# Optimization experiments

Measured on AMD Instinct MI355X. Metric: run time of the kernel, lower is better.

The kernel has to match this reference:

```python
import jax, jax.numpy as jnp
import numpy as np

DEG = [1, 72, 201, 816, 1790, 3756, 6923, 12768, 20286, 31710, 51623, 82296, 124280, 177576, 251115, 326064, 395760, 456840, 506179, 516200, 507003, 493746, 489256, 453936, 420025, 411320, 427761, 420700, 420500, 426780, 414284, 407008, 394053, 360910, 322245, 313704, 282902, 270940, 237783, 209000, 193766, 177870, 162110, 144848, 121230, 112700, 93483, 88512, 72275, 80700, 68799, 56784, 42665, 30996, 25630, 12936, 9804, 8584, 5251, 3480, 3111, 2728, 1890, 1472, 1235, 330, 201, 68, 69, 0, 71]
_d = np.array(DEG, dtype=np.float64)
AVG_LOG = float((np.log(np.arange(len(_d)) + 1.0) * _d).sum() / _d.sum())  # avg_deg['log']

N_NODES, N_EDGES, N_GRAPHS = 10000, 100000, 64
TOWERS, F, F_OUT, N_LAYERS = 5, 75, 15, 4


def setup_inputs() -> dict:
    key = jax.random.key(0)
    ks = jax.random.split(key, 32)
    r = lambda i, shape: jax.random.normal(ks[i], shape, jnp.float32) * 0.1
    return {
        "x": jax.random.normal(ks[0], (N_NODES, 14), jnp.float32),
        "edge_index": jax.random.randint(ks[1], (2, N_EDGES), 0, N_NODES, dtype=jnp.int32),
        "edge_attr": jax.random.normal(ks[2], (N_EDGES, 4), jnp.float32),
        "batch": jnp.sort(jax.random.randint(ks[3], (N_NODES,), 0, N_GRAPHS, dtype=jnp.int32)),
        "node_emb_w": r(4, (14, F)), "node_emb_b": r(5, (F,)),
        "edge_emb_w": r(6, (4, 50)), "edge_emb_b": r(7, (50,)),
        "ee_w": r(8, (N_LAYERS, 50, F)), "ee_b": r(9, (N_LAYERS, F)),
        "pre_w": r(10, (N_LAYERS, TOWERS, 3 * F, F)), "pre_b": r(11, (N_LAYERS, TOWERS, F)),
        "post_w": r(12, (N_LAYERS, TOWERS, 13 * F, F_OUT)), "post_b": r(13, (N_LAYERS, TOWERS, F_OUT)),
        "lin_w": r(14, (N_LAYERS, F, F)), "lin_b": r(15, (N_LAYERS, F)),
        "bn_g": jnp.ones((N_LAYERS, F), jnp.float32), "bn_b": jnp.zeros((N_LAYERS, F), jnp.float32),
        "mlp_w1": r(16, (F, 50)), "mlp_b1": r(17, (50,)),
        "mlp_w2": r(18, (50, 25)), "mlp_b2": r(19, (25,)),
        "mlp_w3": r(20, (25, 1)), "mlp_b3": r(21, (1,)),
    }


def _pna_conv(x, src, dst, ea, ee_w, ee_b, pre_w, pre_b, post_w, post_b, lin_w, lin_b):
    # x: [N, F]; ea: [E, edge_dim]; divide_input=False so every tower sees full F.
    N = x.shape[0]
    e = ea @ ee_w + ee_b                                   # edge_encoder  [E, F]
    h = jnp.concatenate([x[dst], x[src], e], axis=-1)       # [x_i, x_j, e] [E, 3F]
    m = jnp.einsum('ef,tfg->etg', h, pre_w) + pre_b         # per-tower pre nn [E, T, F]
    cnt = jax.ops.segment_sum(jnp.ones((m.shape[0],), x.dtype), dst, N)  # in-degree [N]
    cnt1 = jnp.maximum(cnt, 1.0)[:, None, None]
    mean = jax.ops.segment_sum(m, dst, N) / cnt1
    mean_sq = jax.ops.segment_sum(m * m, dst, N) / cnt1
    std = jnp.sqrt(jax.nn.relu(mean_sq - mean * mean) + 1e-5)
    has = (cnt > 0)[:, None, None]
    mn = jnp.where(has, jax.ops.segment_min(m, dst, N), 0.0)
    mx = jnp.where(has, jax.ops.segment_max(m, dst, N), 0.0)
    agg = jnp.concatenate([mean, mn, mx, std], axis=-1)     # [N, T, 4F]
    scl = jnp.log(cnt1 + 1.0) / AVG_LOG                     # amplification scaler
    out = jnp.concatenate([agg, agg * scl, agg / scl], -1)  # identity/amp/atten [N, T, 12F]
    x_rep = jnp.broadcast_to(x[:, None, :], (N, TOWERS, x.shape[1]))
    out = jnp.concatenate([x_rep, out], axis=-1)            # [N, T, 13F]
    out = jnp.einsum('ntf,tfg->ntg', out, post_w) + post_b  # per-tower post nn [N, T, F_out]
    return out.reshape(N, -1) @ lin_w + lin_b               # [N, F]


def _bn(x, g, b):
    mu = x.mean(0)
    var = x.var(0)  # biased, as torch BatchNorm1d uses for normalization
    return (x - mu) * jax.lax.rsqrt(var + 1e-5) * g + b


def reference(x, edge_index, edge_attr, batch, node_emb_w, node_emb_b, edge_emb_w, edge_emb_b,
              ee_w, ee_b, pre_w, pre_b, post_w, post_b, lin_w, lin_b, bn_g, bn_b,
              mlp_w1, mlp_b1, mlp_w2, mlp_b2, mlp_w3, mlp_b3):
    src, dst = edge_index[0], edge_index[1]
    h = x @ node_emb_w + node_emb_b
    ea = edge_attr @ edge_emb_w + edge_emb_b
    for i in range(N_LAYERS):
        h = jax.nn.relu(_bn(_pna_conv(h, src, dst, ea, ee_w[i], ee_b[i], pre_w[i], pre_b[i],
                                      post_w[i], post_b[i], lin_w[i], lin_b[i]), bn_g[i], bn_b[i]))
    per_atom = h
    g = jax.ops.segment_sum(h, batch, N_GRAPHS)             # global_add_pool [G, F]
    g = jax.nn.relu(g @ mlp_w1 + mlp_b1)
    g = jax.nn.relu(g @ mlp_w2 + mlp_b2)
    g = (g @ mlp_w3 + mlp_b3).reshape(-1)                   # num_out==1 -> view(-1)
    return (g, per_atom)
```

## Files before the change

kernel.cpp:

```cpp
#include <hip/hip_runtime.h>
#include <math.h>

#define NN 10000
#define NE 100000
#define NGR 64
#define NT 5
#define FD 75
#define FOUT 15
#define NLAY 4
#define MAXB 1792

typedef __bf16 bf16;
typedef __bf16 bf16x8 __attribute__((ext_vector_type(8)));
typedef float f32x4 __attribute__((ext_vector_type(4)));

__device__ inline unsigned pk2(float a, float b) {
  bf16 x = (bf16)a, y = (bf16)b;
  unsigned short ux, uy;
  __builtin_memcpy(&ux, &x, 2); __builtin_memcpy(&uy, &y, 2);
  return (unsigned)ux | ((unsigned)uy << 16);
}


__global__ __launch_bounds__(256) void k_node_emb(const float* __restrict__ x,
    const float* __restrict__ w, const float* __restrict__ b, bf16* __restrict__ hbf) {
  int idx = blockIdx.x * 256 + threadIdx.x;
  if (idx >= NN * FD) return;
  int n = idx / FD, f = idx - n * FD;
  float acc = b[f];
#pragma unroll
  for (int k = 0; k < 14; ++k) acc += x[n * 14 + k] * w[k * FD + f];
  hbf[n * 80 + f] = (bf16)acc;
}

__global__ __launch_bounds__(256) void k_edge4(const float* __restrict__ eattr,
    bf16* __restrict__ eabf4) {
  int idx = blockIdx.x * 256 + threadIdx.x;
  if (idx >= NE * 8) return;
  int e = idx >> 3, c = idx & 7;
  eabf4[idx] = (c < 4) ? (bf16)eattr[e * 4 + c] : (bf16)0.f;
}

__global__ __launch_bounds__(256) void k_count(const int* __restrict__ dst, int* __restrict__ deg) {
  int e = blockIdx.x * 256 + threadIdx.x;
  if (e < NE) atomicAdd(&deg[dst[e]], 1);
}

__global__ __launch_bounds__(1024) void k_scan(const int* __restrict__ deg, int* __restrict__ rowptr) {
  __shared__ int buf[1024];
  __shared__ int carry;
  int tid = threadIdx.x;
  if (tid == 0) carry = 0;
  __syncthreads();
  for (int base = 0; base < NN; base += 1024) {
    int i = base + tid;
    int v = (i < NN) ? deg[i] : 0;
    buf[tid] = v;
    __syncthreads();
    for (int off = 1; off < 1024; off <<= 1) {
      int t = (tid >= off) ? buf[tid - off] : 0;
      __syncthreads();
      buf[tid] += t;
      __syncthreads();
    }
    int inc = buf[tid];
    int tot = buf[1023];
    if (i < NN) rowptr[i + 1] = carry + inc;
    __syncthreads();
    if (tid == 0) carry += tot;
    __syncthreads();
  }
  if (tid == 0) rowptr[0] = 0;
}

__global__ __launch_bounds__(256) void k_scl(const int* __restrict__ deg, float* __restrict__ scl,
                                             float* __restrict__ iscl, float inv_avg_log) {
  int n = blockIdx.x * 256 + threadIdx.x;
  if (n >= NN) return;
  float c1 = fmaxf((float)deg[n], 1.f);
  float s = logf(c1 + 1.f) * inv_avg_log;
  scl[n] = s;
  iscl[n] = 1.f / s;
}

__global__ __launch_bounds__(256) void k_scatter(const int* __restrict__ dst, const int* __restrict__ rowptr,
    int* __restrict__ cursor, int* __restrict__ eids) {
  int e = blockIdx.x * 256 + threadIdx.x;
  if (e >= NE) return;
  int d = dst[e];
  int pos = rowptr[d] + atomicAdd(&cursor[d], 1);
  eids[pos] = e;
}

__global__ __launch_bounds__(256) void k_next(const int* __restrict__ rowptr, int* __restrict__ nxt) {
  int n = blockIdx.x * 256 + threadIdx.x;
  if (n >= NN) return;
  int base = rowptr[n];
  int lo = n + 1, hi = min(n + 128, NN);
  while (lo < hi) {
    int mid = (lo + hi + 1) >> 1;
    if (rowptr[mid] - base <= 128) lo = mid; else hi = mid - 1;
  }
  nxt[n] = lo;
}

__global__ __launch_bounds__(1024) void k_walk(const int* __restrict__ nxt,
    int* __restrict__ bstart, int* __restrict__ nblk) {
  __shared__ int lnx[NN];
  int tid = threadIdx.x;
  for (int i = tid; i < NN; i += 1024) lnx[i] = nxt[i];
  __syncthreads();
  if (tid == 0) {
    int b = 0, n = 0;
    while (n < NN && b < MAXB) { bstart[b++] = n; n = lnx[n]; }
    bstart[b] = NN;
    nblk[0] = b;
  }
}


__global__ __launch_bounds__(256) void k_W12(const float* __restrict__ ew,
    const float* __restrict__ ebias, const float* __restrict__ ee_wA, const float* __restrict__ ee_bA,
    float* __restrict__ W12A, float* __restrict__ bcombA) {
  const int l = blockIdx.y;
  const float* ee_w = ee_wA + (size_t)l * 50 * FD;
  const float* ee_b = ee_bA + (size_t)l * FD;
  int idx = blockIdx.x * 256 + threadIdx.x;
  if (idx >= 375) return;
  if (idx < 300) {
    int d = idx / 75, o = idx - d * 75;
    float v = 0.f;
    for (int j = 0; j < 50; ++j) v += ew[d * 50 + j] * ee_w[j * 75 + o];
    W12A[(size_t)l * 300 + idx] = v;
  } else {
    int o = idx - 300;
    float v = ee_b[o];
    for (int j = 0; j < 50; ++j) v += ebias[j] * ee_w[j * 75 + o];
    bcombA[(size_t)l * 80 + o] = v;
  }
}

__global__ __launch_bounds__(256) void k_combine(const float* __restrict__ pre_wA,
    const float* __restrict__ pre_bA, const float* __restrict__ W12A, const float* __restrict__ bcombA,
    bf16* __restrict__ WctA, float* __restrict__ bcA) {
  const int l = blockIdx.y;
  const float* pre_w = pre_wA + (size_t)l * NT * 225 * FD;
  const float* pre_b = pre_bA + (size_t)l * NT * FD;
  const float* W12   = W12A + (size_t)l * 300;
  const float* bcomb = bcombA + (size_t)l * 80;
  bf16* Wct = WctA + (size_t)l * 384 * 192;
  float* bc = bcA + (size_t)l * 384;
  int idx = blockIdx.x * 256 + threadIdx.x;
  if (idx >= 384 * 192) return;
  int c = idx / 192, s = idx - c * 192;
  int t = c / 75, g = c - t * 75;
  int chunk = s >> 6, within = s & 63, sblk = within >> 3, elem = within & 7;
  int lb = sblk ^ (c & 7);
  int k = chunk * 64 + lb * 8 + elem;
  float v = 0.f;
  if (c < 375) {
    if (k < 75)                    v = pre_w[(t * 225 + k) * 75 + g];
    else if (k >= 80 && k < 155)   v = pre_w[(t * 225 + 75 + (k - 80)) * 75 + g];
    else if (k >= 160 && k < 164) {
      int d = k - 160;
      float a = 0.f;
      for (int f2 = 0; f2 < 75; ++f2) a += W12[d * 75 + f2] * pre_w[(t * 225 + 150 + f2) * 75 + g];
      v = a;
    }
  }
  Wct[c * 192 + s] = (bf16)v;
  if (s == 0) {
    float a = 0.f;
    if (c < 375) {
      a = pre_b[t * 75 + g];
      for (int f2 = 0; f2 < 75; ++f2) a += bcomb[f2] * pre_w[(t * 225 + 150 + f2) * 75 + g];
    }
    bc[c] = a;
  }
}

__global__ __launch_bounds__(256) void k_PL(const float* __restrict__ pwA,
    const float* __restrict__ lwA, float* __restrict__ PLA) {
  const int l = blockIdx.y;
  const float* pw = pwA + (size_t)l * NT * 975 * FOUT;
  const float* lw = lwA + (size_t)l * FD * FD;
  float* PL = PLA + (size_t)l * 5 * 975 * 80;
  int idx = blockIdx.x * 256 + threadIdx.x;
  if (idx >= 5 * 975 * 80) return;
  int t = idx / (975 * 80), rem = idx - t * 975 * 80;
  int row = rem / 80, o = rem - row * 80;
  float v = 0.f;
  if (o < 75) {
#pragma unroll
    for (int j = 0; j < 15; ++j)
      v += pw[((size_t)t * 975 + row) * 15 + j] * lw[(t * 15 + j) * 75 + o];
  }
  PL[idx] = v;
}

__global__ __launch_bounds__(256) void k_combine2b(const float* __restrict__ PLA,
    bf16* __restrict__ Wct2A) {
  const int l = blockIdx.y;
  const float* PL = PLA + (size_t)l * 5 * 975 * 80;
  bf16* Wct2 = Wct2A + (size_t)l * 256 * 1664;
  int idx = blockIdx.x * 256 + threadIdx.x;
  if (idx >= 256 * 1664) return;
  int c = idx / 1664, s = idx - c * 1664;
  int chunk = s >> 6, within = s & 63, sblk = within >> 3, elem = within & 7;
  int lb = sblk ^ (c & 7);
  int k = chunk * 64 + lb * 8 + elem;
  int g2 = c / 80, o = c - g2 * 80;
  float val = 0.f;
  if (c < 240 && o < 75) {
    if (k < 75) {
      if (g2 == 0) {
#pragma unroll
        for (int t = 0; t < 5; ++t) val += PL[(t * 975 + k) * 80 + o];
      }
    } else if (k >= 80 && k < 1616) {
      int q = k - 80;
      int si = q / 384, cc = q - si * 384;
      if (cc < 375) {
        int t = cc / 75, g = cc - t * 75;
        int row = 75 + g2 * 300 + si * 75 + g;
        val = PL[((size_t)t * 975 + row) * 80 + o];
      }
    }
  }
  Wct2[(size_t)c * 1664 + s] = (bf16)val;
}

__global__ __launch_bounds__(128) void k_zbias(const float* __restrict__ pbA,
    const float* __restrict__ lwA, const float* __restrict__ lbA, float* __restrict__ zbA) {
  const int l = blockIdx.y;
  const float* pb = pbA + (size_t)l * NT * FOUT;
  const float* lw = lwA + (size_t)l * FD * FD;
  const float* lb = lbA + (size_t)l * FD;
  float* zb = zbA + (size_t)l * 80;
  int o = threadIdx.x;
  if (o >= 80) return;
  float val = 0.f;
  if (o < 75) {
    val = lb[o];
    for (int t = 0; t < 5; ++t)
      for (int j = 0; j < 15; ++j)
        val += pb[t * 15 + j] * lw[(t * 15 + j) * 75 + o];
  }
  zb[o] = val;
}


#define APTR_(g_, pd_, ps_, pe_) \
  ((g_) < 10 ? (pd_) + (g_) * 8 : (g_) < 20 ? (ps_) + ((g_) - 10) * 8 : \
   (g_) < 21 ? (pe_) : zerobuf)

#define LOADA(c_) do { int g_ = (c_) * 8 + slb;                \
    pa0 = *(const uint4*)APTR_(g_, pd0, ps0, pe0);             \
    pa1 = *(const uint4*)APTR_(g_, pd1, ps1, pe1);             \
    pa2 = *(const uint4*)APTR_(g_, pd2, ps2, pe2);             \
    pa3 = *(const uint4*)APTR_(g_, pd3, ps3, pe3); } while (0)

#define LOADB(ntb_, c_) do {                                                      \
    const bf16* wp_ = Wct + (size_t)((ntb_) + sr) * 192 + (c_) * 64 + slb * 8;    \
    pq0 = *(const uint4*)(wp_ + 0 * 6144);                                        \
    pq1 = *(const uint4*)(wp_ + 1 * 6144);                                        \
    pq2 = *(const uint4*)(wp_ + 2 * 6144);                                        \
    pq3 = *(const uint4*)(wp_ + 3 * 6144); } while (0)

#define STORE_AB() do { int swz_ = (slb ^ (sr & 7)) << 4;       \
    *(uint4*)(As + (0 * 32 + sr) * 128 + swz_) = pa0;           \
    *(uint4*)(As + (1 * 32 + sr) * 128 + swz_) = pa1;           \
    *(uint4*)(As + (2 * 32 + sr) * 128 + swz_) = pa2;           \
    *(uint4*)(As + (3 * 32 + sr) * 128 + swz_) = pa3;           \
    *(uint4*)(Bs + (0 * 32 + sr) * 128 + (slb << 4)) = pq0;     \
    *(uint4*)(Bs + (1 * 32 + sr) * 128 + (slb << 4)) = pq1;     \
    *(uint4*)(Bs + (2 * 32 + sr) * 128 + (slb << 4)) = pq2;     \
    *(uint4*)(Bs + (3 * 32 + sr) * 128 + (slb << 4)) = pq3; } while (0)

__global__ __launch_bounds__(256) void k_pre_fused(
    const bf16* __restrict__ hbf, const bf16* __restrict__ eabf4,
    const int* __restrict__ eids, const int* __restrict__ srcA, const int* __restrict__ dstA,
    const int* __restrict__ rowptr, const int* __restrict__ bstart, const int* __restrict__ nblk,
    const bf16* __restrict__ Wct, const float* __restrict__ bc,
    const bf16* __restrict__ zerobuf, bf16* __restrict__ aggbf2) {
  __shared__ __align__(16) unsigned char smem[33792];
  unsigned char* As = smem;
  unsigned char* Bs = smem + 16384;
  bf16* m_lds = (bf16*)smem;
  __shared__ const bf16* pDl[128];
  __shared__ const bf16* pSl[128];
  __shared__ const bf16* pEl[128];
  __shared__ int nodeRows[129];
  __shared__ int nq[5];

  const int b = blockIdx.x;
  if (b >= nblk[0]) return;
  const int ntb = blockIdx.y * 128;
  const int tid = threadIdx.x;
  const int n0b = bstart[b], n1b = bstart[b + 1];
  const int rbase = rowptr[n0b];
  const int nrows = rowptr[n1b] - rbase;
  const int nnod = n1b - n0b;

  if (tid == 0) { nq[0] = 0; nq[1] = 0; nq[2] = 0; nq[3] = 0; nq[4] = nnod; }
  if (tid < 128) {
    if (tid < nrows) {
      int e = eids[rbase + tid];
      pDl[tid] = hbf + dstA[e] * 80;
      pSl[tid] = hbf + srcA[e] * 80;
      pEl[tid] = eabf4 + e * 8;
    } else { pDl[tid] = zerobuf; pSl[tid] = zerobuf; pEl[tid] = zerobuf; }
  }
  if (tid <= nnod) nodeRows[tid] = rowptr[n0b + tid] - rbase;
  __syncthreads();
  if (tid < nnod) {
#pragma unroll
    for (int q = 1; q <= 3; ++q) {
      int target = (nrows * q) >> 2;
      if (nodeRows[tid] < target && nodeRows[tid + 1] >= target) nq[q] = tid + 1;
    }
  }

  const int lane = tid & 63;
  const int wave = tid >> 6;
  const int wr = wave >> 1, wc = wave & 1;
  const int l15 = lane & 15, l4 = lane >> 4;
  const int sr = tid >> 3, slb = tid & 7;

  const bf16 *pd0 = pDl[sr],      *ps0 = pSl[sr],      *pe0 = pEl[sr];
  const bf16 *pd1 = pDl[32 + sr], *ps1 = pSl[32 + sr], *pe1 = pEl[32 + sr];
  const bf16 *pd2 = pDl[64 + sr], *ps2 = pSl[64 + sr], *pe2 = pEl[64 + sr];
  const bf16 *pd3 = pDl[96 + sr], *ps3 = pSl[96 + sr], *pe3 = pEl[96 + sr];

  f32x4 acc[4][4];
  f32x4 zv = {0.f, 0.f, 0.f, 0.f};
#pragma unroll
  for (int i = 0; i < 4; ++i)
#pragma unroll
    for (int j = 0; j < 4; ++j) acc[i][j] = zv;

  uint4 pa0, pa1, pa2, pa3, pq0, pq1, pq2, pq3;
  LOADA(0); LOADB(ntb, 0);

#pragma unroll
  for (int c = 0; c < 3; ++c) {
    STORE_AB();
    __syncthreads();
    if (c < 2) { LOADA(c + 1); LOADB(ntb, c + 1); }
#pragma unroll
    for (int kk = 0; kk < 2; ++kk) {
      int kb = kk * 4 + l4;
      bf16x8 af[4], bfv[4];
#pragma unroll
      for (int i = 0; i < 4; ++i) {
        int row = wr * 64 + i * 16 + l15;
        af[i] = *(const bf16x8*)(As + row * 128 + ((kb ^ (row & 7)) << 4));
      }
#pragma unroll
      for (int j = 0; j < 4; ++j) {
        int col = wc * 64 + j * 16 + l15;
        bfv[j] = *(const bf16x8*)(Bs + col * 128 + ((kb ^ (col & 7)) << 4));
      }
#pragma unroll
      for (int i = 0; i < 4; ++i)
#pragma unroll
        for (int j = 0; j < 4; ++j)
          acc[i][j] = __builtin_amdgcn_mfma_f32_16x16x32_bf16(af[i], bfv[j], acc[i][j], 0, 0, 0);
    }
    __syncthreads();
  }

  float bcv[4];
#pragma unroll
  for (int j = 0; j < 4; ++j) bcv[j] = bc[ntb + wc * 64 + j * 16 + l15];
#pragma unroll
  for (int i = 0; i < 4; ++i) {
    int R = wr * 64 + i * 16 + l4 * 4;
#pragma unroll
    for (int j = 0; j < 4; ++j) {
      int col = wc * 64 + j * 16 + l15;
#pragma unroll
      for (int q = 0; q < 4; ++q)
        m_lds[(R + q) * 132 + col] = (bf16)(acc[i][j][q] + bcv[j]);
    }
  }
  __syncthreads();

  {
    const int cp = tid & 63;
    const int qq = tid >> 6;
    const unsigned char* mb = (const unsigned char*)m_lds;
    for (int i = nq[qq]; i < nq[qq + 1]; ++i) {
      int ra = nodeRows[i], rb2 = nodeRows[i + 1];
      float s0 = 0.f, q0 = 0.f, a0 = INFINITY, b0 = -INFINITY;
      float s1 = 0.f, q1 = 0.f, a1 = INFINITY, b1 = -INFINITY;
      for (int r = ra; r < rb2; ++r) {
        unsigned u = *(const unsigned*)(mb + r * 264 + cp * 4);
        float v0 = __uint_as_float(u << 16);
        float v1 = __uint_as_float(u & 0xffff0000u);
        s0 += v0; q0 += v0 * v0; a0 = fminf(a0, v0); b0 = fmaxf(b0, v0);
        s1 += v1; q1 += v1 * v1; a1 = fminf(a1, v1); b1 = fmaxf(b1, v1);
      }
      int d = rb2 - ra;
      float inv = 1.f / ((d > 0) ? (float)d : 1.f);
      float m0 = s0 * inv, m1 = s1 * inv;
      float sd0 = sqrtf(fmaxf(q0 * inv - m0 * m0, 0.f) + 1e-5f);
      float sd1 = sqrtf(fmaxf(q1 * inv - m1 * m1, 0.f) + 1e-5f);
      if (d == 0) { a0 = 0.f; b0 = 0.f; a1 = 0.f; b1 = 0.f; }
      bf16* ag = aggbf2 + (size_t)(n0b + i) * 1536 + ntb + cp * 2;
      *(unsigned*)(ag)        = pk2(m0, m1);
      *(unsigned*)(ag + 384)  = pk2(a0, a1);
      *(unsigned*)(ag + 768)  = pk2(b0, b1);
      *(unsigned*)(ag + 1152) = pk2(sd0, sd1);
    }
  }
}


#define APG_(g_) ((nA >= NN || (g_) >= 202) ? zerobuf : \
    ((g_) < 10 ? hbf + nA * 80 + (g_) * 8 : aggbf2 + (size_t)nA * 1536 + ((g_) - 10) * 8))

#define LOADP4(c_) do {                                                 \
    int gA_ = (c_) * 16 + slb;                                          \
    pa0 = *(const uint4*)APG_(gA_);                                     \
    pa1 = *(const uint4*)APG_(gA_ + 8);                                 \
    int ko_ = (c_) * 128 + slb * 8;                                     \
    pb0 = *(const uint4*)(pc0 + ko_);                                   \
    pb1 = *(const uint4*)(pc0 + ko_ + 64);                              \
    pb2 = *(const uint4*)(pc1 + ko_);                                   \
    pb3 = *(const uint4*)(pc1 + ko_ + 64);                              \
    pb4 = *(const uint4*)(pc2 + ko_);                                   \
    pb5 = *(const uint4*)(pc2 + ko_ + 64);                              \
    pb6 = *(const uint4*)(pc3 + ko_);                                   \
    pb7 = *(const uint4*)(pc3 + ko_ + 64);                              \
  } while (0)

__global__ __launch_bounds__(256) void k_post4(const bf16* __restrict__ hbf,
    const bf16* __restrict__ aggbf2, const bf16* __restrict__ Wct2,
    const float* __restrict__ zb, const float* __restrict__ scl, const float* __restrict__ iscl,
    const bf16* __restrict__ zerobuf, float* __restrict__ z, float* __restrict__ stat_raw_l) {
  __shared__ __align__(16) unsigned char smem[40960];
  unsigned char* As = smem;
  unsigned char* Bs = smem + 8192;
  float* Ps = (float*)smem;
  __shared__ float sclS[32], isclS[32];
  const int n0 = blockIdx.x * 32;
  const int y  = blockIdx.y;
  const int tid = threadIdx.x;
  const int lane = tid & 63, wave = tid >> 6;
  const int l15 = lane & 15, l4 = lane >> 4;
  const int sr = tid >> 3, slb = tid & 7;
  const int nA = n0 + sr;

  const bf16 *pc0, *pc1, *pc2, *pc3;
  {
    int c0 = sr, c1 = sr + 32, c2 = sr + 64, c3 = sr + 96;
    int l0 = (c0 / 40) * 80 + y * 40 + (c0 % 40);
    int l1 = (c1 / 40) * 80 + y * 40 + (c1 % 40);
    int l2 = (c2 / 40) * 80 + y * 40 + (c2 % 40);
    int l3 = (c3 < 120) ? ((c3 / 40) * 80 + y * 40 + (c3 % 40)) : 0;
    pc0 = Wct2 + (size_t)l0 * 1664;
    pc1 = Wct2 + (size_t)l1 * 1664;
    pc2 = Wct2 + (size_t)l2 * 1664;
    pc3 = Wct2 + (size_t)l3 * 1664;
  }
  if (tid < 32) {
    int n = n0 + tid;
    sclS[tid] = (n < NN) ? scl[n] : 0.f;
    isclS[tid] = (n < NN) ? iscl[n] : 0.f;
  }

  f32x4 acc[2][2];
  f32x4 zvv = {0.f, 0.f, 0.f, 0.f};
#pragma unroll
  for (int i = 0; i < 2; ++i)
#pragma unroll
    for (int j = 0; j < 2; ++j) acc[i][j] = zvv;

  uint4 pa0, pa1, pb0, pb1, pb2, pb3, pb4, pb5, pb6, pb7;
  LOADP4(0);
  for (int c = 0; c < 13; ++c) {
    {
      int s1_ = (slb ^ (sr & 7)) << 4;
      *(uint4*)(As + sr * 256 + s1_) = pa0;
      *(uint4*)(As + sr * 256 + s1_ + 128) = pa1;
      *(uint4*)(Bs + (sr)      * 256 + (slb << 4)) = pb0;
      *(uint4*)(Bs + (sr)      * 256 + (slb << 4) + 128) = pb1;
      *(uint4*)(Bs + (sr + 32) * 256 + (slb << 4)) = pb2;
      *(uint4*)(Bs + (sr + 32) * 256 + (slb << 4) + 128) = pb3;
      *(uint4*)(Bs + (sr + 64) * 256 + (slb << 4)) = pb4;
      *(uint4*)(Bs + (sr + 64) * 256 + (slb << 4) + 128) = pb5;
      *(uint4*)(Bs + (sr + 96) * 256 + (slb << 4)) = pb6;
      *(uint4*)(Bs + (sr + 96) * 256 + (slb << 4) + 128) = pb7;
    }
    __syncthreads();
    if (c < 12) LOADP4(c + 1);
#pragma unroll
    for (int kk = 0; kk < 4; ++kk) {
      int kb = kk * 4 + l4;
      bf16x8 af[2], bv[2];
#pragma unroll
      for (int i = 0; i < 2; ++i) {
        int row = i * 16 + l15;
        af[i] = *(const bf16x8*)(As + row * 256 + (((kb & 8) | ((kb & 7) ^ (row & 7))) << 4));
      }
#pragma unroll
      for (int j = 0; j < 2; ++j) {
        int cidx = wave * 32 + j * 16 + l15;
        bv[j] = *(const bf16x8*)(Bs + cidx * 256 + (((kb & 8) | ((kb & 7) ^ (cidx & 7))) << 4));
      }
#pragma unroll
      for (int i = 0; i < 2; ++i)
#pragma unroll
        for (int j = 0; j < 2; ++j)
          acc[i][j] = __builtin_amdgcn_mfma_f32_16x16x32_bf16(af[i], bv[j], acc[i][j], 0, 0, 0);
    }
    __syncthreads();
  }

#pragma unroll
  for (int i = 0; i < 2; ++i) {
#pragma unroll
    for (int j = 0; j < 2; ++j) {
      int cidx = wave * 32 + j * 16 + l15;
#pragma unroll
      for (int q = 0; q < 4; ++q)
        Ps[(i * 16 + l4 * 4 + q) * 132 + cidx] = acc[i][j][q];
    }
  }
  __syncthreads();

  float v0_, v1_, v2_, v3_, v4_;
  int r0_, r1_, r2_, r3_, r4_, f0_, f1_, f2_, f3_, f4_;
#define EPI(t_, vv_, rr_, ff_) do {                                           \
    int idx_ = tid + (t_) * 256;                                              \
    rr_ = idx_ / 40; ff_ = idx_ - rr_ * 40;                                   \
    int n_ = n0 + rr_, zc_ = y * 40 + ff_;                                    \
    float v_ = 0.f;                                                           \
    if (n_ < NN && zc_ < 75) {                                                \
      v_ = Ps[rr_ * 132 + ff_] + sclS[rr_] * Ps[rr_ * 132 + 40 + ff_]         \
         + isclS[rr_] * Ps[rr_ * 132 + 80 + ff_] + zb[zc_];                   \
      z[n_ * 75 + zc_] = v_;                                                  \
    }                                                                         \
    vv_ = v_;                                                                 \
  } while (0)
  EPI(0, v0_, r0_, f0_); EPI(1, v1_, r1_, f1_); EPI(2, v2_, r2_, f2_);
  EPI(3, v3_, r3_, f3_); EPI(4, v4_, r4_, f4_);
#undef EPI
  __syncthreads();
  Ps[r0_ * 132 + f0_] = v0_;
  Ps[r1_ * 132 + f1_] = v1_;
  Ps[r2_ * 132 + f2_] = v2_;
  Ps[r3_ * 132 + f3_] = v3_;
  Ps[r4_ * 132 + f4_] = v4_;
  __syncthreads();
  if (tid < 40) {
    int zc = y * 40 + tid;
    if (zc < 75) {
      float s = 0.f, s2 = 0.f;
#pragma unroll
      for (int r = 0; r < 32; ++r) {
        float v = Ps[r * 132 + tid];
        s += v; s2 += v * v;
      }
      atomicAdd(&stat_raw_l[zc], s);
      atomicAdd(&stat_raw_l[75 + zc], s2);
    }
  }
}

__global__ __launch_bounds__(256) void k_bnapply(const float* __restrict__ z,
    const float* __restrict__ stat_raw, const float* __restrict__ g, const float* __restrict__ b,
    float* __restrict__ outF, bf16* __restrict__ hbf) {
  int idx = blockIdx.x * 256 + threadIdx.x;
  if (idx >= NN * FD) return;
  int n = idx / FD, f = idx - n * FD;
  float mu = stat_raw[f] * (1.f / NN);
  float var = stat_raw[75 + f] * (1.f / NN) - mu * mu;
  var = fmaxf(var, 0.f);
  float rs = 1.f / sqrtf(var + 1e-5f);
  float v = (z[idx] - mu) * rs * g[f] + b[f];
  v = fmaxf(v, 0.f);
  if (outF) outF[idx] = v;
  hbf[n * 80 + f] = (bf16)v;
}

__global__ __launch_bounds__(256) void k_pool(const float* __restrict__ h, const int* __restrict__ batch,
                                              float* __restrict__ gpool) {
  int idx = blockIdx.x * 256 + threadIdx.x;
  if (idx >= NN * FD) return;
  int n = idx / FD, f = idx - n * FD;
  atomicAdd(&gpool[batch[n] * FD + f], h[idx]);
}

__global__ __launch_bounds__(256) void k_mlp(const float* __restrict__ gpool,
    const float* __restrict__ w1, const float* __restrict__ b1,
    const float* __restrict__ w2, const float* __restrict__ b2,
    const float* __restrict__ w3, const float* __restrict__ b3,
    float* __restrict__ out) {
  __shared__ float G[NGR * FD];
  __shared__ float G1[NGR * 50];
  __shared__ float G2[NGR * 25];
  int tid = threadIdx.x;
  for (int i = tid; i < NGR * FD; i += 256) G[i] = gpool[i];
  __syncthreads();
  for (int i = tid; i < NGR * 50; i += 256) {
    int r = i / 50, c = i - r * 50;
    float a = b1[c];
    for (int k = 0; k < FD; ++k) a += G[r * FD + k] * w1[k * 50 + c];
    G1[i] = fmaxf(a, 0.f);
  }
  __syncthreads();
  for (int i = tid; i < NGR * 25; i += 256) {
    int r = i / 25, c = i - r * 25;
    float a = b2[c];
    for (int k = 0; k < 50; ++k) a += G1[r * 50 + k] * w2[k * 25 + c];
    G2[i] = fmaxf(a, 0.f);
  }
  __syncthreads();
  if (tid < NGR) {
    float a = b3[0];
    for (int k = 0; k < 25; ++k) a += G2[tid * 25 + k] * w3[k];
    out[tid] = a;
  }
}


extern "C" void kernel_launch(void* const* d_in, const int* in_sizes, int n_in,
                              void* d_out, int out_size, void* d_ws, size_t ws_size,
                              hipStream_t stream) {
  (void)in_sizes; (void)n_in; (void)out_size; (void)ws_size;
  const float* x      = (const float*)d_in[0];
  const int*   eidx   = (const int*)  d_in[1];
  const float* eattr  = (const float*)d_in[2];
  const int*   batch  = (const int*)  d_in[3];
  const float* nw     = (const float*)d_in[4];
  const float* nb     = (const float*)d_in[5];
  const float* ew     = (const float*)d_in[6];
  const float* ebias  = (const float*)d_in[7];
  const float* ee_w   = (const float*)d_in[8];
  const float* ee_b   = (const float*)d_in[9];
  const float* pre_w  = (const float*)d_in[10];
  const float* pre_b  = (const float*)d_in[11];
  const float* post_w = (const float*)d_in[12];
  const float* post_b = (const float*)d_in[13];
  const float* lin_w  = (const float*)d_in[14];
  const float* lin_b  = (const float*)d_in[15];
  const float* bn_g   = (const float*)d_in[16];
  const float* bn_b   = (const float*)d_in[17];
  const float* w1 = (const float*)d_in[18];
  const float* b1 = (const float*)d_in[19];
  const float* w2 = (const float*)d_in[20];
  const float* b2 = (const float*)d_in[21];
  const float* w3 = (const float*)d_in[22];
  const float* b3 = (const float*)d_in[23];

  const int* srcA = eidx;
  const int* dstA = eidx + NE;

  char* base = (char*)d_ws;
  size_t off = 0;
  auto alloc = [&](size_t bytes) -> char* {
    char* p = base + off;
    off = (off + bytes + 255) & ~(size_t)255;
    return p;
  };
  bf16*  hbf    = (bf16*) alloc((size_t)NN * 80 * 2);
  bf16*  eabf4  = (bf16*) alloc((size_t)NE * 8 * 2);
  bf16*  aggbf2 = (bf16*) alloc((size_t)NN * 1536 * 2);
  float* z      = (float*)alloc((size_t)NN * FD * 4);
  bf16*  WctA   = (bf16*) alloc((size_t)NLAY * 384 * 192 * 2);
  float* bcA    = (float*)alloc((size_t)NLAY * 384 * 4);
  bf16*  Wct2A  = (bf16*) alloc((size_t)NLAY * 256 * 1664 * 2);
  float* zbA    = (float*)alloc((size_t)NLAY * 80 * 4);
  float* PLA    = (float*)alloc((size_t)NLAY * 5 * 975 * 80 * 4);
  float* W12A   = (float*)alloc((size_t)NLAY * 300 * 4);
  float* bcombA = (float*)alloc((size_t)NLAY * 80 * 4);
  float* scl    = (float*)alloc(NN * 4);
  float* iscl   = (float*)alloc(NN * 4);
  int*   deg    = (int*)alloc(NN * 4);
  int*   rowptr = (int*)alloc((NN + 1) * 4);
  int*   cursor = (int*)alloc(NN * 4);
  int*   eids   = (int*)alloc(NE * 4);
  int*   nxt    = (int*)alloc(NN * 4);
  int*   bstart = (int*)alloc((MAXB + 1) * 4);
  int*   nblk   = (int*)alloc(16);
  float* stat_all = (float*)alloc((size_t)NLAY * 160 * 4);
  float* gpool  = (float*)alloc(NGR * FD * 4);
  bf16*  zerobuf = (bf16*)alloc(256);

  static const int DEG_TAB[71] = {1, 72, 201, 816, 1790, 3756, 6923, 12768, 20286, 31710,
    51623, 82296, 124280, 177576, 251115, 326064, 395760, 456840, 506179, 516200, 507003,
    493746, 489256, 453936, 420025, 411320, 427761, 420700, 420500, 426780, 414284, 407008,
    394053, 360910, 322245, 313704, 282902, 270940, 237783, 209000, 193766, 177870, 162110,
    144848, 121230, 112700, 93483, 88512, 72275, 80700, 68799, 56784, 42665, 30996, 25630,
    12936, 9804, 8584, 5251, 3480, 3111, 2728, 1890, 1472, 1235, 330, 201, 68, 69, 0, 71};
  double num = 0.0, den = 0.0;
  for (int i = 0; i < 71; ++i) { num += log((double)i + 1.0) * DEG_TAB[i]; den += DEG_TAB[i]; }
  float inv_avg_log = (float)(den / num);

  hipMemsetAsync(deg, 0, NN * 4, stream);
  hipMemsetAsync(cursor, 0, NN * 4, stream);
  hipMemsetAsync(gpool, 0, NGR * FD * 4, stream);
  hipMemsetAsync(stat_all, 0, (size_t)NLAY * 160 * 4, stream);
  hipMemsetAsync(zerobuf, 0, 256, stream);

  k_node_emb<<<(NN * FD + 255) / 256, 256, 0, stream>>>(x, nw, nb, hbf);
  k_edge4<<<(NE * 8 + 255) / 256, 256, 0, stream>>>(eattr, eabf4);
  k_count<<<(NE + 255) / 256, 256, 0, stream>>>(dstA, deg);
  k_scan<<<1, 1024, 0, stream>>>(deg, rowptr);
  k_scl<<<(NN + 255) / 256, 256, 0, stream>>>(deg, scl, iscl, inv_avg_log);
  k_scatter<<<(NE + 255) / 256, 256, 0, stream>>>(dstA, rowptr, cursor, eids);
  k_next<<<(NN + 255) / 256, 256, 0, stream>>>(rowptr, nxt);
  k_walk<<<1, 1024, 0, stream>>>(nxt, bstart, nblk);

  {
    dim3 gw(2, NLAY);
    k_W12<<<gw, 256, 0, stream>>>(ew, ebias, ee_w, ee_b, W12A, bcombA);
    dim3 gc((384 * 192 + 255) / 256, NLAY);
    k_combine<<<gc, 256, 0, stream>>>(pre_w, pre_b, W12A, bcombA, WctA, bcA);
    dim3 gp((5 * 975 * 80 + 255) / 256, NLAY);
    k_PL<<<gp, 256, 0, stream>>>(post_w, lin_w, PLA);
    dim3 g2((256 * 1664 + 255) / 256, NLAY);
    k_combine2b<<<g2, 256, 0, stream>>>(PLA, Wct2A);
    dim3 gz(1, NLAY);
    k_zbias<<<gz, 128, 0, stream>>>(post_b, lin_w, lin_b, zbA);
  }

  float* outp = (float*)d_out;
  for (int l = 0; l < NLAY; ++l) {
    dim3 gpref(MAXB, 3);
    k_pre_fused<<<gpref, 256, 0, stream>>>(hbf, eabf4, eids, srcA, dstA, rowptr, bstart, nblk,
        WctA + (size_t)l * 384 * 192, bcA + (size_t)l * 384, zerobuf, aggbf2);
    dim3 gpost((NN + 31) / 32, 2);
    k_post4<<<gpost, 256, 0, stream>>>(hbf, aggbf2, Wct2A + (size_t)l * 256 * 1664,
        zbA + (size_t)l * 80, scl, iscl, zerobuf, z, stat_all + (size_t)l * 160);
    float* wdst = (l == NLAY - 1) ? (outp + NGR) : nullptr;
    k_bnapply<<<(NN * FD + 255) / 256, 256, 0, stream>>>(z, stat_all + (size_t)l * 160,
        bn_g + (size_t)l * FD, bn_b + (size_t)l * FD, wdst, hbf);
  }

  k_pool<<<(NN * FD + 255) / 256, 256, 0, stream>>>(outp + NGR, batch, gpool);
  k_mlp<<<1, 256, 0, stream>>>(gpool, w1, b1, w2, b2, w3, b3, outp);
}
```

Measured before the change: 568.6 us.

## Load gathered A operands directly from global into MFMA registers, skip LDS staging

The pre-aggregation GEMM no longer stages the gathered dst/src/edge rows through shared memory. Each lane computes byte offsets into hbf and the edge buffer and loads its bf16x8 A fragments straight from global memory. B tiles are double-buffered in LDS instead, which removes one barrier and the LDS round-trip for A. A pad-zeroing kernel is added so the 75..79 columns of hbf are zero, since the K layout now reads those padding slots directly. The trade-off is uncoalesced per-lane global loads for A, and edge offsets are relative to hbf, which relies on unsigned offset arithmetic.

Result: faster. 545.0 us (-4.2%).

```diff
diff --git a/kernel.cpp b/kernel.cpp
--- a/kernel.cpp
+++ b/kernel.cpp
@@ -31,6 +31,13 @@
 #pragma unroll
   for (int k = 0; k < 14; ++k) acc += x[n * 14 + k] * w[k * FD + f];
   hbf[n * 80 + f] = (bf16)acc;
+}
+
+__global__ __launch_bounds__(256) void k_hpad(bf16* __restrict__ hbf) {
+  int idx = blockIdx.x * 256 + threadIdx.x;
+  if (idx >= NN * 5) return;
+  int n = idx / 5, f = 75 + idx % 5;
+  hbf[n * 80 + f] = (bf16)0.f;
 }
 
 __global__ __launch_bounds__(256) void k_edge4(const float* __restrict__ eattr,
@@ -250,16 +257,6 @@
 }
 
 
-#define APTR_(g_, pd_, ps_, pe_) \
-  ((g_) < 10 ? (pd_) + (g_) * 8 : (g_) < 20 ? (ps_) + ((g_) - 10) * 8 : \
-   (g_) < 21 ? (pe_) : zerobuf)
-
-#define LOADA(c_) do { int g_ = (c_) * 8 + slb;                \
-    pa0 = *(const uint4*)APTR_(g_, pd0, ps0, pe0);             \
-    pa1 = *(const uint4*)APTR_(g_, pd1, ps1, pe1);             \
-    pa2 = *(const uint4*)APTR_(g_, pd2, ps2, pe2);             \
-    pa3 = *(const uint4*)APTR_(g_, pd3, ps3, pe3); } while (0)
-
 #define LOADB(ntb_, c_) do {                                                      \
     const bf16* wp_ = Wct + (size_t)((ntb_) + sr) * 192 + (c_) * 64 + slb * 8;    \
     pq0 = *(const uint4*)(wp_ + 0 * 6144);                                        \
@@ -267,29 +264,51 @@
     pq2 = *(const uint4*)(wp_ + 2 * 6144);                                        \
     pq3 = *(const uint4*)(wp_ + 3 * 6144); } while (0)
 
-#define STORE_AB() do { int swz_ = (slb ^ (sr & 7)) << 4;       \
-    *(uint4*)(As + (0 * 32 + sr) * 128 + swz_) = pa0;           \
-    *(uint4*)(As + (1 * 32 + sr) * 128 + swz_) = pa1;           \
-    *(uint4*)(As + (2 * 32 + sr) * 128 + swz_) = pa2;           \
-    *(uint4*)(As + (3 * 32 + sr) * 128 + swz_) = pa3;           \
-    *(uint4*)(Bs + (0 * 32 + sr) * 128 + (slb << 4)) = pq0;     \
-    *(uint4*)(Bs + (1 * 32 + sr) * 128 + (slb << 4)) = pq1;     \
-    *(uint4*)(Bs + (2 * 32 + sr) * 128 + (slb << 4)) = pq2;     \
-    *(uint4*)(Bs + (3 * 32 + sr) * 128 + (slb << 4)) = pq3; } while (0)
+#define STOREB(BS_) do {                                          \
+    *(uint4*)((BS_) + (0 * 32 + sr) * 128 + (slb << 4)) = pq0;    \
+    *(uint4*)((BS_) + (1 * 32 + sr) * 128 + (slb << 4)) = pq1;    \
+    *(uint4*)((BS_) + (2 * 32 + sr) * 128 + (slb << 4)) = pq2;    \
+    *(uint4*)((BS_) + (3 * 32 + sr) * 128 + (slb << 4)) = pq3; } while (0)
+
+#define DO_KK(BS_, KB_, A0_, A1_, A2_, A3_) do {                         \
+    bf16x8 af0 = *(const bf16x8*)(A0_);                                  \
+    bf16x8 af1 = *(const bf16x8*)(A1_);                                  \
+    bf16x8 af2 = *(const bf16x8*)(A2_);                                  \
+    bf16x8 af3 = *(const bf16x8*)(A3_);                                  \
+    const unsigned char* bp_ = (BS_) + (((KB_) ^ (l15 & 7)) << 4) + wc * 8192 + l15 * 128; \
+    bf16x8 bv0 = *(const bf16x8*)(bp_ + 0 * 2048);                       \
+    bf16x8 bv1 = *(const bf16x8*)(bp_ + 1 * 2048);                       \
+    bf16x8 bv2 = *(const bf16x8*)(bp_ + 2 * 2048);                       \
+    bf16x8 bv3 = *(const bf16x8*)(bp_ + 3 * 2048);                       \
+    acc[0][0] = __builtin_amdgcn_mfma_f32_16x16x32_bf16(af0, bv0, acc[0][0], 0, 0, 0); \
+    acc[1][0] = __builtin_amdgcn_mfma_f32_16x16x32_bf16(af1, bv0, acc[1][0], 0, 0, 0); \
+    acc[2][0] = __builtin_amdgcn_mfma_f32_16x16x32_bf16(af2, bv0, acc[2][0], 0, 0, 0); \
+    acc[3][0] = __builtin_amdgcn_mfma_f32_16x16x32_bf16(af3, bv0, acc[3][0], 0, 0, 0); \
+    acc[0][1] = __builtin_amdgcn_mfma_f32_16x16x32_bf16(af0, bv1, acc[0][1], 0, 0, 0); \
+    acc[1][1] = __builtin_amdgcn_mfma_f32_16x16x32_bf16(af1, bv1, acc[1][1], 0, 0, 0); \
+    acc[2][1] = __builtin_amdgcn_mfma_f32_16x16x32_bf16(af2, bv1, acc[2][1], 0, 0, 0); \
+    acc[3][1] = __builtin_amdgcn_mfma_f32_16x16x32_bf16(af3, bv1, acc[3][1], 0, 0, 0); \
+    acc[0][2] = __builtin_amdgcn_mfma_f32_16x16x32_bf16(af0, bv2, acc[0][2], 0, 0, 0); \
+    acc[1][2] = __builtin_amdgcn_mfma_f32_16x16x32_bf16(af1, bv2, acc[1][2], 0, 0, 0); \
+    acc[2][2] = __builtin_amdgcn_mfma_f32_16x16x32_bf16(af2, bv2, acc[2][2], 0, 0, 0); \
+    acc[3][2] = __builtin_amdgcn_mfma_f32_16x16x32_bf16(af3, bv2, acc[3][2], 0, 0, 0); \
+    acc[0][3] = __builtin_amdgcn_mfma_f32_16x16x32_bf16(af0, bv3, acc[0][3], 0, 0, 0); \
+    acc[1][3] = __builtin_amdgcn_mfma_f32_16x16x32_bf16(af1, bv3, acc[1][3], 0, 0, 0); \
+    acc[2][3] = __builtin_amdgcn_mfma_f32_16x16x32_bf16(af2, bv3, acc[2][3], 0, 0, 0); \
+    acc[3][3] = __builtin_amdgcn_mfma_f32_16x16x32_bf16(af3, bv3, acc[3][3], 0, 0, 0); \
+  } while (0)
 
 __global__ __launch_bounds__(256) void k_pre_fused(
-    const bf16* __restrict__ hbf, const bf16* __restrict__ eabf4,
-    const int* __restrict__ eids, const int* __restrict__ srcA, const int* __restrict__ dstA,
+    const bf16* __restrict__ hbf, const int* __restrict__ eids,
+    const int* __restrict__ srcA, const int* __restrict__ dstA,
     const int* __restrict__ rowptr, const int* __restrict__ bstart, const int* __restrict__ nblk,
     const bf16* __restrict__ Wct, const float* __restrict__ bc,
-    const bf16* __restrict__ zerobuf, bf16* __restrict__ aggbf2) {
+    bf16* __restrict__ aggbf2, unsigned eoff_base) {
   __shared__ __align__(16) unsigned char smem[33792];
-  unsigned char* As = smem;
-  unsigned char* Bs = smem + 16384;
+  unsigned char* Bs0 = smem;
+  unsigned char* Bs1 = smem + 16384;
   bf16* m_lds = (bf16*)smem;
-  __shared__ const bf16* pDl[128];
-  __shared__ const bf16* pSl[128];
-  __shared__ const bf16* pEl[128];
+  __shared__ unsigned dOffL[128], sOffL[128], eOffL[128];
   __shared__ int nodeRows[129];
   __shared__ int nq[5];
 
@@ -304,12 +323,10 @@
 
   if (tid == 0) { nq[0] = 0; nq[1] = 0; nq[2] = 0; nq[3] = 0; nq[4] = nnod; }
   if (tid < 128) {
-    if (tid < nrows) {
-      int e = eids[rbase + tid];
-      pDl[tid] = hbf + dstA[e] * 80;
-      pSl[tid] = hbf + srcA[e] * 80;
-      pEl[tid] = eabf4 + e * 8;
-    } else { pDl[tid] = zerobuf; pSl[tid] = zerobuf; pEl[tid] = zerobuf; }
+    int e = (tid < nrows) ? eids[rbase + tid] : 0;
+    dOffL[tid] = (unsigned)(dstA[e] * 160);
+    sOffL[tid] = (unsigned)(srcA[e] * 160);
+    eOffL[tid] = eoff_base + (unsigned)(e * 16);
   }
   if (tid <= nnod) nodeRows[tid] = rowptr[n0b + tid] - rbase;
   __syncthreads();
@@ -327,10 +344,11 @@
   const int l15 = lane & 15, l4 = lane >> 4;
   const int sr = tid >> 3, slb = tid & 7;
 
-  const bf16 *pd0 = pDl[sr],      *ps0 = pSl[sr],      *pe0 = pEl[sr];
-  const bf16 *pd1 = pDl[32 + sr], *ps1 = pSl[32 + sr], *pe1 = pEl[32 + sr];
-  const bf16 *pd2 = pDl[64 + sr], *ps2 = pSl[64 + sr], *pe2 = pEl[64 + sr];
-  const bf16 *pd3 = pDl[96 + sr], *ps3 = pSl[96 + sr], *pe3 = pEl[96 + sr];
+  const unsigned char* hb = (const unsigned char*)hbf;
+  const int ar = wr * 64 + l15;
+  const unsigned dof0 = dOffL[ar], dof1 = dOffL[ar + 16], dof2 = dOffL[ar + 32], dof3 = dOffL[ar + 48];
+  const unsigned sof0 = sOffL[ar], sof1 = sOffL[ar + 16], sof2 = sOffL[ar + 32], sof3 = sOffL[ar + 48];
+  const unsigned eof0 = eOffL[ar], eof1 = eOffL[ar + 16], eof2 = eOffL[ar + 32], eof3 = eOffL[ar + 48];
 
   f32x4 acc[4][4];
   f32x4 zv = {0.f, 0.f, 0.f, 0.f};
@@ -339,36 +357,32 @@
 #pragma unroll
     for (int j = 0; j < 4; ++j) acc[i][j] = zv;
 
-  uint4 pa0, pa1, pa2, pa3, pq0, pq1, pq2, pq3;
-  LOADA(0); LOADB(ntb, 0);
-
-#pragma unroll
-  for (int c = 0; c < 3; ++c) {
-    STORE_AB();
-    __syncthreads();
-    if (c < 2) { LOADA(c + 1); LOADB(ntb, c + 1); }
-#pragma unroll
-    for (int kk = 0; kk < 2; ++kk) {
-      int kb = kk * 4 + l4;
-      bf16x8 af[4], bfv[4];
-#pragma unroll
-      for (int i = 0; i < 4; ++i) {
-        int row = wr * 64 + i * 16 + l15;
-        af[i] = *(const bf16x8*)(As + row * 128 + ((kb ^ (row & 7)) << 4));
-      }
-#pragma unroll
-      for (int j = 0; j < 4; ++j) {
-        int col = wc * 64 + j * 16 + l15;
-        bfv[j] = *(const bf16x8*)(Bs + col * 128 + ((kb ^ (col & 7)) << 4));
-      }
-#pragma unroll
-      for (int i = 0; i < 4; ++i)
-#pragma unroll
-        for (int j = 0; j < 4; ++j)
-          acc[i][j] = __builtin_amdgcn_mfma_f32_16x16x32_bf16(af[i], bfv[j], acc[i][j], 0, 0, 0);
-    }
-    __syncthreads();
-  }
+  uint4 pq0, pq1, pq2, pq3;
+  LOADB(ntb, 0);
+
+  STOREB(Bs0);
+  __syncthreads();
+  LOADB(ntb, 1);
+  DO_KK(Bs0, l4,     hb + dof0 + l4 * 16, hb + dof1 + l4 * 16, hb + dof2 + l4 * 16, hb + dof3 + l4 * 16);
+  DO_KK(Bs0, 4 + l4, hb + dof0 + 64 + l4 * 16, hb + dof1 + 64 + l4 * 16, hb + dof2 + 64 + l4 * 16, hb + dof3 + 64 + l4 * 16);
+
+  STOREB(Bs1);
+  __syncthreads();
+  LOADB(ntb, 2);
+  {
+    unsigned o0 = (l4 < 2) ? (dof0 + 128 + l4 * 16) : (sof0 + (l4 - 2) * 16);
+    unsigned o1 = (l4 < 2) ? (dof1 + 128 + l4 * 16) : (sof1 + (l4 - 2) * 16);
+    unsigned o2 = (l4 < 2) ? (dof2 + 128 + l4 * 16) : (sof2 + (l4 - 2) * 16);
+    unsigned o3 = (l4 < 2) ? (dof3 + 128 + l4 * 16) : (sof3 + (l4 - 2) * 16);
+    DO_KK(Bs1, l4, hb + o0, hb + o1, hb + o2, hb + o3);
+  }
+  DO_KK(Bs1, 4 + l4, hb + sof0 + 32 + l4 * 16, hb + sof1 + 32 + l4 * 16, hb + sof2 + 32 + l4 * 16, hb + sof3 + 32 + l4 * 16);
+
+  STOREB(Bs0);
+  __syncthreads();
+  DO_KK(Bs0, l4, hb + sof0 + 96 + l4 * 16, hb + sof1 + 96 + l4 * 16, hb + sof2 + 96 + l4 * 16, hb + sof3 + 96 + l4 * 16);
+  DO_KK(Bs0, 4 + l4, hb + eof0 + l4 * 16, hb + eof1 + l4 * 16, hb + eof2 + l4 * 16, hb + eof3 + l4 * 16);
+  __syncthreads();
 
   float bcv[4];
 #pragma unroll
@@ -666,7 +680,7 @@
     return p;
   };
   bf16*  hbf    = (bf16*) alloc((size_t)NN * 80 * 2);
-  bf16*  eabf4  = (bf16*) alloc((size_t)NE * 8 * 2);
+  bf16*  eabf4  = (bf16*) alloc((size_t)NE * 8 * 2 + 64);
   bf16*  aggbf2 = (bf16*) alloc((size_t)NN * 1536 * 2);
   float* z      = (float*)alloc((size_t)NN * FD * 4);
   bf16*  WctA   = (bf16*) alloc((size_t)NLAY * 384 * 192 * 2);
@@ -689,6 +703,8 @@
   float* gpool  = (float*)alloc(NGR * FD * 4);
   bf16*  zerobuf = (bf16*)alloc(256);
 
+  const unsigned eoff_base = (unsigned)((char*)eabf4 - (char*)hbf);
+
   static const int DEG_TAB[71] = {1, 72, 201, 816, 1790, 3756, 6923, 12768, 20286, 31710,
     51623, 82296, 124280, 177576, 251115, 326064, 395760, 456840, 506179, 516200, 507003,
     493746, 489256, 453936, 420025, 411320, 427761, 420700, 420500, 426780, 414284, 407008,
@@ -706,6 +722,7 @@
   hipMemsetAsync(zerobuf, 0, 256, stream);
 
   k_node_emb<<<(NN * FD + 255) / 256, 256, 0, stream>>>(x, nw, nb, hbf);
+  k_hpad<<<(NN * 5 + 255) / 256, 256, 0, stream>>>(hbf);
   k_edge4<<<(NE * 8 + 255) / 256, 256, 0, stream>>>(eattr, eabf4);
   k_count<<<(NE + 255) / 256, 256, 0, stream>>>(dstA, deg);
   k_scan<<<1, 1024, 0, stream>>>(deg, rowptr);
@@ -730,8 +747,8 @@
   float* outp = (float*)d_out;
   for (int l = 0; l < NLAY; ++l) {
     dim3 gpref(MAXB, 3);
-    k_pre_fused<<<gpref, 256, 0, stream>>>(hbf, eabf4, eids, srcA, dstA, rowptr, bstart, nblk,
-        WctA + (size_t)l * 384 * 192, bcA + (size_t)l * 384, zerobuf, aggbf2);
+    k_pre_fused<<<gpref, 256, 0, stream>>>(hbf, eids, srcA, dstA, rowptr, bstart, nblk,
+        WctA + (size_t)l * 384 * 192, bcA + (size_t)l * 384, aggbf2, eoff_base);
     dim3 gpost((NN + 31) / 32, 2);
     k_post4<<<gpost, 256, 0, stream>>>(hbf, aggbf2, Wct2A + (size_t)l * 256 * 1664,
         zbA + (size_t)l * 80, scl, iscl, zerobuf, z, stat_all + (size_t)l * 160);
```
